# Optimization experiments

Hardware: AMD Instinct MI355X
Metric: run time of the kernel (lower is better)

The kernel has to match this reference:

```python
import jax, jax.numpy as jnp
import numpy as np

H = 1024       # hidden_size
I = 1024       # intermediate_size
E = 16         # num_experts
K = 4          # experts_per_token
LIMIT = 7.0    # swiglu_limit
ALPHA = 1.702  # swiglu alpha
EPS = 1e-5     # rmsnorm eps


def setup_inputs() -> dict:
    key = jax.random.key(0)
    ks = jax.random.split(key, 8)
    x = jax.random.normal(ks[0], (2, 512, H), dtype=jnp.float32)
    norm_scale = jnp.ones((H,), dtype=jnp.float32)
    wg = jax.random.normal(ks[1], (H, E), dtype=jnp.float32) * 0.02
    bg = jax.random.normal(ks[2], (E,), dtype=jnp.float32) * 0.02
    w1 = jax.random.normal(ks[3], (E, H, 2 * I), dtype=jnp.float32) * 0.02
    b1 = jax.random.normal(ks[4], (E, 2 * I), dtype=jnp.float32) * 0.02
    w2 = jax.random.normal(ks[5], (E, I, H), dtype=jnp.float32) * 0.02
    b2 = jax.random.normal(ks[6], (E, H), dtype=jnp.float32) * 0.02
    return {"x": x, "norm_scale": norm_scale, "wg": wg, "bg": bg,
            "w1": w1, "b1": b1, "w2": w2, "b2": b2}


def reference(x, norm_scale, wg, bg, w1, b1, w2, b2):
    shape = x.shape
    xf = x.reshape(-1, shape[-1])                                   # [T, H]
    # RMSNorm (float32 math)
    xn = xf * jax.lax.rsqrt(jnp.mean(xf * xf, axis=-1, keepdims=True) + EPS) * norm_scale
    # router logits + top-k with softmax over selected logits
    logits = xn @ wg + bg                                           # [T, E]
    vals, idx = jax.lax.top_k(logits, K)                            # [T, K]
    gates = jax.nn.softmax(vals, axis=-1)                           # [T, K]
    # dense [T, E] gate matrix (exactly equivalent to gather/scatter grouped GEMM)
    gate_full = jnp.einsum('tke,tk->te', jax.nn.one_hot(idx, E, dtype=gates.dtype), gates)
    # expert FFN 1 + fused swiglu (interleaved gate/linear pairs)
    h = jnp.einsum('th,ehd->etd', xn, w1) + b1[:, None, :]          # [E, T, 2I]
    a = jnp.minimum(h[..., ::2], LIMIT)                             # gate branch
    b = jnp.clip(h[..., 1::2], -LIMIT, LIMIT)                       # linear branch
    s = a * jax.nn.sigmoid(ALPHA * a) * (b + 1.0)                   # [E, T, I]
    # expert FFN 2; gamma (gate) scales the full epilogue incl. bias
    y = jnp.einsum('eti,eih->eth', s, w2) + b2[:, None, :]          # [E, T, H]
    t = jnp.einsum('eth,te->th', y, gate_full)                      # scatter-combine
    return x + t.reshape(shape)
```

## Files before the change

kernel.cpp:

```cpp
#include <hip/hip_runtime.h>

#define NH 1024
#define NI2 2048
#define NI 1024
#define NE 16
#define NT 1024

static constexpr float LIMITF = 7.0f;
static constexpr float ALPHAF = 1.702f;
static constexpr float EPSF = 1e-5f;

typedef short bf16x8 __attribute__((ext_vector_type(8)));
typedef float f32x16 __attribute__((ext_vector_type(16)));

__device__ __forceinline__ unsigned short f2bf(float f) {
  unsigned int u = __builtin_bit_cast(unsigned int, f);
  u = (u + 0x7FFFu + ((u >> 16) & 1u)) >> 16;
  return (unsigned short)u;
}

__global__ __launch_bounds__(256) void k_init(const float* __restrict__ x,
                                              float* __restrict__ out) {
  int i = blockIdx.x * 256 + threadIdx.x;
  reinterpret_cast<float4*>(out)[i] = reinterpret_cast<const float4*>(x)[i];
}

__global__ __launch_bounds__(256) void k_norm_router(
    const float* __restrict__ x, const float* __restrict__ nsc,
    const float* __restrict__ wg, const float* __restrict__ bg,
    unsigned short* __restrict__ xn, int* __restrict__ topk_idx,
    float* __restrict__ topk_gate, int* __restrict__ counts) {
  int t = blockIdx.x;
  int tid = threadIdx.x;
  int wave = tid >> 6, lane = tid & 63;

  float4 v = reinterpret_cast<const float4*>(x + (size_t)t * NH)[tid];
  float ss = v.x * v.x + v.y * v.y + v.z * v.z + v.w * v.w;
  for (int off = 32; off; off >>= 1) ss += __shfl_xor(ss, off);

  __shared__ float red[4];
  __shared__ float redl[4][16];
  __shared__ float logits_s[16];
  if (lane == 0) red[wave] = ss;
  __syncthreads();
  float tot = red[0] + red[1] + red[2] + red[3];
  float r = rsqrtf(tot * (1.0f / NH) + EPSF);

  float4 sc = reinterpret_cast<const float4*>(nsc)[tid];
  float xv[4];
  xv[0] = v.x * r * sc.x;
  xv[1] = v.y * r * sc.y;
  xv[2] = v.z * r * sc.z;
  xv[3] = v.w * r * sc.w;

  ushort4 o;
  o.x = f2bf(xv[0]); o.y = f2bf(xv[1]); o.z = f2bf(xv[2]); o.w = f2bf(xv[3]);
  reinterpret_cast<ushort4*>(xn + (size_t)t * NH)[tid] = o;

  float acc[16];
#pragma unroll
  for (int e = 0; e < 16; e++) acc[e] = 0.f;
  int hbase = tid * 4;
#pragma unroll
  for (int i = 0; i < 4; i++) {
    const float4* wr = reinterpret_cast<const float4*>(wg + (size_t)(hbase + i) * NE);
#pragma unroll
    for (int j = 0; j < 4; j++) {
      float4 w = wr[j];
      acc[j * 4 + 0] += xv[i] * w.x;
      acc[j * 4 + 1] += xv[i] * w.y;
      acc[j * 4 + 2] += xv[i] * w.z;
      acc[j * 4 + 3] += xv[i] * w.w;
    }
  }
#pragma unroll
  for (int e = 0; e < 16; e++)
    for (int off = 32; off; off >>= 1) acc[e] += __shfl_xor(acc[e], off);
  if (lane == 0) {
#pragma unroll
    for (int e = 0; e < 16; e++) redl[wave][e] = acc[e];
  }
  __syncthreads();
  if (tid < 16)
    logits_s[tid] = redl[0][tid] + redl[1][tid] + redl[2][tid] + redl[3][tid] + bg[tid];
  __syncthreads();

  if (tid == 0) {
    float vals[16];
#pragma unroll
    for (int e = 0; e < 16; e++) vals[e] = logits_s[e];
    int sel[4]; float sv[4];
    unsigned used = 0;
    for (int k = 0; k < 4; k++) {
      float best = -1e30f; int bi = 0;
      for (int e = 0; e < 16; e++) {
        if (!((used >> e) & 1u) && vals[e] > best) { best = vals[e]; bi = e; }
      }
      used |= 1u << bi; sel[k] = bi; sv[k] = best;
    }
    float g[4], ssum = 0.f;
    for (int k = 0; k < 4; k++) { g[k] = __expf(sv[k] - sv[0]); ssum += g[k]; }
    for (int k = 0; k < 4; k++) {
      topk_idx[t * 4 + k] = sel[k];
      topk_gate[t * 4 + k] = g[k] / ssum;
      atomicAdd(&counts[sel[k]], 1);
    }
  }
}

__global__ void k_scan(const int* __restrict__ counts, int* __restrict__ offsets,
                       int* __restrict__ cursor) {
  if (blockIdx.x == 0 && threadIdx.x == 0) {
    int o = 0;
    for (int e = 0; e < NE; e++) { offsets[e] = o; cursor[e] = o; o += counts[e]; }
  }
}

__global__ __launch_bounds__(256) void k_fill(const int* __restrict__ topk_idx,
                                              const float* __restrict__ topk_gate,
                                              int* __restrict__ cursor,
                                              int* __restrict__ rows_tok,
                                              float* __restrict__ rows_gate) {
  int idx = blockIdx.x * 256 + threadIdx.x;
  if (idx >= NT * 4) return;
  int e = topk_idx[idx];
  int slot = atomicAdd(&cursor[e], 1);
  rows_tok[slot] = idx >> 2;
  rows_gate[slot] = topk_gate[idx];
}

__global__ __launch_bounds__(256, 4) void k_ffn1(
    const unsigned short* __restrict__ xn, const float* __restrict__ w1,
    const float* __restrict__ b1, const int* __restrict__ counts,
    const int* __restrict__ offsets, const int* __restrict__ rows_tok,
    unsigned short* __restrict__ s_buf) {
  int e = blockIdx.y;
  int cnt = counts[e];
  if (cnt == 0) return;
  int n0 = blockIdx.x * 32;
  int rowbase = offsets[e];
  int tid = threadIdx.x;

  __shared__ __align__(16) unsigned short lds_b[2 * 16 * 32 * 8];

  const float* w1e = w1 + (size_t)e * (NH * NI2) + n0;
  int col = tid & 31, kc8 = tid >> 5;

  int lane = tid & 63, wave = tid >> 6;
  int lrow = lane & 31, khalf = lane >> 5;
  float bias = b1[(size_t)e * NI2 + n0 + lrow];
  int parity = lrow & 1;

  for (int m0 = 0; m0 < cnt; m0 += 256) {
    int tb0 = m0 + wave * 32;
    int tb1 = m0 + 128 + wave * 32;
    bool dual = (m0 + 128) < cnt;
    int tok0 = rows_tok[rowbase + min(tb0 + lrow, cnt - 1)];
    const unsigned short* a0p = xn + (size_t)tok0 * NH;
    const unsigned short* a1p = a0p;
    if (dual) {
      int tok1 = rows_tok[rowbase + min(tb1 + lrow, cnt - 1)];
      a1p = xn + (size_t)tok1 * NH;
    }

    f32x16 acc0 = {0.f,0.f,0.f,0.f,0.f,0.f,0.f,0.f,0.f,0.f,0.f,0.f,0.f,0.f,0.f,0.f};
    f32x16 acc1 = {0.f,0.f,0.f,0.f,0.f,0.f,0.f,0.f,0.f,0.f,0.f,0.f,0.f,0.f,0.f,0.f};

    __syncthreads();
#pragma unroll
    for (int half = 0; half < 2; half++) {
      int kcz = kc8 + half * 8;
      int kb = kcz * 8;
      float f[8];
#pragma unroll
      for (int j = 0; j < 8; j++) f[j] = w1e[(size_t)(kb + j) * NI2 + col];
      unsigned pk[4];
#pragma unroll
      for (int j = 0; j < 4; j++)
        pk[j] = (unsigned)f2bf(f[2 * j]) | ((unsigned)f2bf(f[2 * j + 1]) << 16);
      *reinterpret_cast<uint4*>(&lds_b[(size_t)(kcz * 32 + col) * 8]) =
          *reinterpret_cast<const uint4*>(pk);
    }
    __syncthreads();

    int buf = 0;
    for (int kt = 0; kt < 8; kt++) {
      float fst[2][8];
      if (kt < 7) {
        int k0n = (kt + 1) * 128;
#pragma unroll
        for (int half = 0; half < 2; half++) {
          int kb = (kc8 + half * 8) * 8;
#pragma unroll
          for (int j = 0; j < 8; j++)
            fst[half][j] = w1e[(size_t)(k0n + kb + j) * NI2 + col];
        }
      }
      const unsigned short* ab0 = a0p + kt * 128 + khalf * 8;
      const unsigned short* ab1 = a1p + kt * 128 + khalf * 8;
#pragma unroll
      for (int k2 = 0; k2 < 8; k2++) {
        bf16x8 bv = *reinterpret_cast<const bf16x8*>(
            &lds_b[(size_t)(((buf * 16) + k2 * 2 + khalf) * 32 + lrow) * 8]);
        bf16x8 av0 = *reinterpret_cast<const bf16x8*>(ab0 + k2 * 16);
        acc0 = __builtin_amdgcn_mfma_f32_32x32x16_bf16(av0, bv, acc0, 0, 0, 0);
        if (dual) {
          bf16x8 av1 = *reinterpret_cast<const bf16x8*>(ab1 + k2 * 16);
          acc1 = __builtin_amdgcn_mfma_f32_32x32x16_bf16(av1, bv, acc1, 0, 0, 0);
        }
      }
      if (kt < 7) {
        int nb = buf ^ 1;
#pragma unroll
        for (int half = 0; half < 2; half++) {
          int kcz = kc8 + half * 8;
          unsigned pk[4];
#pragma unroll
          for (int j = 0; j < 4; j++)
            pk[j] = (unsigned)f2bf(fst[half][2 * j]) |
                    ((unsigned)f2bf(fst[half][2 * j + 1]) << 16);
          *reinterpret_cast<uint4*>(
              &lds_b[(size_t)((nb * 16 + kcz) * 32 + col) * 8]) =
              *reinterpret_cast<const uint4*>(pk);
        }
        __syncthreads();
        buf = nb;
      }
    }

#pragma unroll
    for (int t2 = 0; t2 < 2; t2++) {
      if (t2 == 1 && !dual) break;
      f32x16 acc = t2 ? acc1 : acc0;
      int tb = t2 ? tb1 : tb0;
#pragma unroll
      for (int reg = 0; reg < 16; reg++) {
        float v = acc[reg] + bias;
        float p = __shfl_xor(v, 1);
        int row = (reg & 3) + 8 * (reg >> 2) + 4 * khalf;
        int m = tb + row;
        if (!parity && m < cnt) {
          float aa = fminf(v, LIMITF);
          float bb = fminf(fmaxf(p, -LIMITF), LIMITF);
          float sig = 1.0f / (1.0f + __expf(-ALPHAF * aa));
          float sval = aa * sig * (bb + 1.0f);
          s_buf[(size_t)(rowbase + m) * NI + ((n0 + lrow) >> 1)] = f2bf(sval);
        }
      }
    }
  }
}

__global__ __launch_bounds__(256, 4) void k_ffn2(
    const unsigned short* __restrict__ s_buf, const float* __restrict__ w2,
    const float* __restrict__ b2, const int* __restrict__ counts,
    const int* __restrict__ offsets, const int* __restrict__ rows_tok,
    const float* __restrict__ rows_gate, float* __restrict__ out) {
  int e = blockIdx.y;
  int cnt = counts[e];
  if (cnt == 0) return;
  int n0 = blockIdx.x * 32;
  int ks = blockIdx.z;
  int rowbase = offsets[e];
  int tid = threadIdx.x;

  __shared__ __align__(16) unsigned short lds_b[2 * 16 * 32 * 8];

  const float* w2e = w2 + (size_t)e * (NI * NH) + n0;
  int col = tid & 31, kc8 = tid >> 5;
  int kbase = ks * 512;

  int lane = tid & 63, wave = tid >> 6;
  int lrow = lane & 31, khalf = lane >> 5;
  float b2v = (ks == 0) ? b2[(size_t)e * NH + n0 + lrow] : 0.f;

  for (int m0 = 0; m0 < cnt; m0 += 256) {
    int tb0 = m0 + wave * 32;
    int tb1 = m0 + 128 + wave * 32;
    bool dual = (m0 + 128) < cnt;
    int r0 = rowbase + min(tb0 + lrow, cnt - 1);
    const unsigned short* a0p = s_buf + (size_t)r0 * NI + kbase;
    const unsigned short* a1p = a0p;
    if (dual) {
      int r1 = rowbase + min(tb1 + lrow, cnt - 1);
      a1p = s_buf + (size_t)r1 * NI + kbase;
    }

    f32x16 acc0 = {0.f,0.f,0.f,0.f,0.f,0.f,0.f,0.f,0.f,0.f,0.f,0.f,0.f,0.f,0.f,0.f};
    f32x16 acc1 = {0.f,0.f,0.f,0.f,0.f,0.f,0.f,0.f,0.f,0.f,0.f,0.f,0.f,0.f,0.f,0.f};

    __syncthreads();
#pragma unroll
    for (int half = 0; half < 2; half++) {
      int kcz = kc8 + half * 8;
      int kb = kcz * 8;
      float f[8];
#pragma unroll
      for (int j = 0; j < 8; j++)
        f[j] = w2e[(size_t)(kbase + kb + j) * NH + col];
      unsigned pk[4];
#pragma unroll
      for (int j = 0; j < 4; j++)
        pk[j] = (unsigned)f2bf(f[2 * j]) | ((unsigned)f2bf(f[2 * j + 1]) << 16);
      *reinterpret_cast<uint4*>(&lds_b[(size_t)(kcz * 32 + col) * 8]) =
          *reinterpret_cast<const uint4*>(pk);
    }
    __syncthreads();

    int buf = 0;
    for (int kt = 0; kt < 4; kt++) {
      float fst[2][8];
      if (kt < 3) {
        int k0n = kbase + (kt + 1) * 128;
#pragma unroll
        for (int half = 0; half < 2; half++) {
          int kb = (kc8 + half * 8) * 8;
#pragma unroll
          for (int j = 0; j < 8; j++)
            fst[half][j] = w2e[(size_t)(k0n + kb + j) * NH + col];
        }
      }
      const unsigned short* ab0 = a0p + kt * 128 + khalf * 8;
      const unsigned short* ab1 = a1p + kt * 128 + khalf * 8;
#pragma unroll
      for (int k2 = 0; k2 < 8; k2++) {
        bf16x8 bv = *reinterpret_cast<const bf16x8*>(
            &lds_b[(size_t)(((buf * 16) + k2 * 2 + khalf) * 32 + lrow) * 8]);
        bf16x8 av0 = *reinterpret_cast<const bf16x8*>(ab0 + k2 * 16);
        acc0 = __builtin_amdgcn_mfma_f32_32x32x16_bf16(av0, bv, acc0, 0, 0, 0);
        if (dual) {
          bf16x8 av1 = *reinterpret_cast<const bf16x8*>(ab1 + k2 * 16);
          acc1 = __builtin_amdgcn_mfma_f32_32x32x16_bf16(av1, bv, acc1, 0, 0, 0);
        }
      }
      if (kt < 3) {
        int nb = buf ^ 1;
#pragma unroll
        for (int half = 0; half < 2; half++) {
          int kcz = kc8 + half * 8;
          unsigned pk[4];
#pragma unroll
          for (int j = 0; j < 4; j++)
            pk[j] = (unsigned)f2bf(fst[half][2 * j]) |
                    ((unsigned)f2bf(fst[half][2 * j + 1]) << 16);
          *reinterpret_cast<uint4*>(
              &lds_b[(size_t)((nb * 16 + kcz) * 32 + col) * 8]) =
              *reinterpret_cast<const uint4*>(pk);
        }
        __syncthreads();
        buf = nb;
      }
    }

#pragma unroll
    for (int t2 = 0; t2 < 2; t2++) {
      if (t2 == 1 && !dual) break;
      f32x16 acc = t2 ? acc1 : acc0;
      int tb = t2 ? tb1 : tb0;
#pragma unroll
      for (int reg = 0; reg < 16; reg++) {
        int row = (reg & 3) + 8 * (reg >> 2) + 4 * khalf;
        int m = tb + row;
        if (m < cnt) {
          int rr = rowbase + m;
          int tok = rows_tok[rr];
          float g = rows_gate[rr];
          atomicAdd(&out[(size_t)tok * NH + n0 + lrow], g * (acc[reg] + b2v));
        }
      }
    }
  }
}

extern "C" void kernel_launch(void* const* d_in, const int* in_sizes, int n_in,
                              void* d_out, int out_size, void* d_ws, size_t ws_size,
                              hipStream_t stream) {
  const float* x   = (const float*)d_in[0];
  const float* nsc = (const float*)d_in[1];
  const float* wg  = (const float*)d_in[2];
  const float* bg  = (const float*)d_in[3];
  const float* w1  = (const float*)d_in[4];
  const float* b1  = (const float*)d_in[5];
  const float* w2  = (const float*)d_in[6];
  const float* b2  = (const float*)d_in[7];
  float* out = (float*)d_out;
  char* ws = (char*)d_ws;

  int*   counts    = (int*)(ws + 0);
  int*   offsets   = (int*)(ws + 64);
  int*   cursor    = (int*)(ws + 128);
  int*   topk_idx  = (int*)(ws + 1024);
  float* topk_gate = (float*)(ws + 1024 + 16384);
  int*   rows_tok  = (int*)(ws + 1024 + 32768);
  float* rows_gate = (float*)(ws + 1024 + 49152);
  unsigned short* xn    = (unsigned short*)(ws + 131072);
  unsigned short* s_buf = (unsigned short*)(ws + 4 * 1024 * 1024);

  hipMemsetAsync(ws, 0, 256, stream);
  k_init<<<NT * NH / 1024, 256, 0, stream>>>(x, out);
  k_norm_router<<<NT, 256, 0, stream>>>(x, nsc, wg, bg, xn, topk_idx, topk_gate,
                                        counts);
  k_scan<<<1, 64, 0, stream>>>(counts, offsets, cursor);
  k_fill<<<16, 256, 0, stream>>>(topk_idx, topk_gate, cursor, rows_tok, rows_gate);
  k_ffn1<<<dim3(NI2 / 32, NE), 256, 0, stream>>>(xn, w1, b1, counts, offsets,
                                                 rows_tok, s_buf);
  k_ffn2<<<dim3(NH / 32, NE, 2), 256, 0, stream>>>(s_buf, w2, b2, counts, offsets,
                                                   rows_tok, rows_gate, out);
}
```

Baseline: 472.6 us.

## Pack routed activations into MFMA-fragment tiles and replace atomic scatter with combine

Pads each expert's row range to multiples of 32 and gathers routed xn rows into a pre-swizzled fragment layout. Each lane then loads contiguous 16-byte A operands instead of gathering from scattered token rows. FFN1 writes the swiglu output through LDS into the same packed layout. FFN2 drops its split-K and atomicAdd scatter, writing gated per-slot outputs that a separate combine kernel sums with the residual. This removes the atomics and the init copy, at the cost of extra pack, pad and combine kernels plus intermediate buffer traffic and less FFN2 parallelism.

After: 457.8 us. 1.03x faster.

```diff
diff --git a/kernel.cpp b/kernel.cpp
--- a/kernel.cpp
+++ b/kernel.cpp
@@ -5,6 +5,8 @@
 #define NI 1024
 #define NE 16
 #define NT 1024
+#define MAXSLOT 4608
+#define MAXTILE 144
 
 static constexpr float LIMITF = 7.0f;
 static constexpr float ALPHAF = 1.702f;
@@ -17,12 +19,6 @@
   unsigned int u = __builtin_bit_cast(unsigned int, f);
   u = (u + 0x7FFFu + ((u >> 16) & 1u)) >> 16;
   return (unsigned short)u;
-}
-
-__global__ __launch_bounds__(256) void k_init(const float* __restrict__ x,
-                                              float* __restrict__ out) {
-  int i = blockIdx.x * 256 + threadIdx.x;
-  reinterpret_cast<float4*>(out)[i] = reinterpret_cast<const float4*>(x)[i];
 }
 
 __global__ __launch_bounds__(256) void k_norm_router(
@@ -112,7 +108,11 @@
                        int* __restrict__ cursor) {
   if (blockIdx.x == 0 && threadIdx.x == 0) {
     int o = 0;
-    for (int e = 0; e < NE; e++) { offsets[e] = o; cursor[e] = o; o += counts[e]; }
+    for (int e = 0; e < NE; e++) {
+      offsets[e] = o; cursor[e] = o;
+      o += (counts[e] + 31) & ~31;
+    }
+    offsets[NE] = o;
   }
 }
 
@@ -120,28 +120,62 @@
                                               const float* __restrict__ topk_gate,
                                               int* __restrict__ cursor,
                                               int* __restrict__ rows_tok,
-                                              float* __restrict__ rows_gate) {
+                                              float* __restrict__ rows_gate,
+                                              int* __restrict__ slot_of) {
   int idx = blockIdx.x * 256 + threadIdx.x;
   if (idx >= NT * 4) return;
   int e = topk_idx[idx];
   int slot = atomicAdd(&cursor[e], 1);
   rows_tok[slot] = idx >> 2;
   rows_gate[slot] = topk_gate[idx];
+  slot_of[idx] = slot;
+}
+
+__global__ void k_pad(const int* __restrict__ counts, const int* __restrict__ offsets,
+                      int* __restrict__ rows_tok, float* __restrict__ rows_gate) {
+  int e = blockIdx.x;
+  int start = offsets[e] + counts[e];
+  int end = offsets[e] + ((counts[e] + 31) & ~31);
+  int s = start + (int)threadIdx.x;
+  if (s < end) { rows_tok[s] = 0; rows_gate[s] = 0.f; }
+}
+
+__global__ __launch_bounds__(256) void k_pack(
+    const unsigned short* __restrict__ xn, const int* __restrict__ rows_tok,
+    const int* __restrict__ offsets, unsigned short* __restrict__ apack) {
+  int tile = blockIdx.x;
+  if (tile * 32 >= offsets[NE]) return;
+  int tid = threadIdx.x;
+  int r = tid >> 3, s = tid & 7;
+  int tok = rows_tok[tile * 32 + r];
+  const unsigned short* src = xn + (size_t)tok * NH;
+  int i0 = blockIdx.y * 4;
+#pragma unroll
+  for (int i = 0; i < 4; i++) {
+    int k0 = (i0 + i) * 64 + s * 8;
+    uint4 v = *reinterpret_cast<const uint4*>(src + k0);
+    int kstep = k0 >> 4;
+    int kh = s & 1;
+    *reinterpret_cast<uint4*>(
+        apack + ((size_t)(tile * 64 + kstep) * 64 + kh * 32 + r) * 8) = v;
+  }
 }
 
 __global__ __launch_bounds__(256, 4) void k_ffn1(
-    const unsigned short* __restrict__ xn, const float* __restrict__ w1,
+    const unsigned short* __restrict__ apack, const float* __restrict__ w1,
     const float* __restrict__ b1, const int* __restrict__ counts,
-    const int* __restrict__ offsets, const int* __restrict__ rows_tok,
-    unsigned short* __restrict__ s_buf) {
+    const int* __restrict__ offsets, unsigned short* __restrict__ spack) {
   int e = blockIdx.y;
   int cnt = counts[e];
   if (cnt == 0) return;
-  int n0 = blockIdx.x * 32;
-  int rowbase = offsets[e];
+  int ntiles = (cnt + 31) >> 5;
+  int tilebase = offsets[e] >> 5;
+  int bx = blockIdx.x;
+  int n0 = bx * 32;
   int tid = threadIdx.x;
 
   __shared__ __align__(16) unsigned short lds_b[2 * 16 * 32 * 8];
+  __shared__ __align__(16) unsigned short lds_t[4][32 * 16];
 
   const float* w1e = w1 + (size_t)e * (NH * NI2) + n0;
   int col = tid & 31, kc8 = tid >> 5;
@@ -151,17 +185,14 @@
   float bias = b1[(size_t)e * NI2 + n0 + lrow];
   int parity = lrow & 1;
 
-  for (int m0 = 0; m0 < cnt; m0 += 256) {
-    int tb0 = m0 + wave * 32;
-    int tb1 = m0 + 128 + wave * 32;
-    bool dual = (m0 + 128) < cnt;
-    int tok0 = rows_tok[rowbase + min(tb0 + lrow, cnt - 1)];
-    const unsigned short* a0p = xn + (size_t)tok0 * NH;
-    const unsigned short* a1p = a0p;
-    if (dual) {
-      int tok1 = rows_tok[rowbase + min(tb1 + lrow, cnt - 1)];
-      a1p = xn + (size_t)tok1 * NH;
-    }
+  for (int c0 = 0; c0 < ntiles; c0 += 8) {
+    int t0 = c0 + wave, t1 = c0 + wave + 4;
+    bool v0 = t0 < ntiles, v1 = t1 < ntiles;
+    int at0 = v0 ? t0 : 0, at1 = v1 ? t1 : 0;
+    const unsigned short* a0 =
+        apack + ((size_t)(tilebase + at0) * 64 * 64 + lane) * 8;
+    const unsigned short* a1 =
+        apack + ((size_t)(tilebase + at1) * 64 * 64 + lane) * 8;
 
     f32x16 acc0 = {0.f,0.f,0.f,0.f,0.f,0.f,0.f,0.f,0.f,0.f,0.f,0.f,0.f,0.f,0.f,0.f};
     f32x16 acc1 = {0.f,0.f,0.f,0.f,0.f,0.f,0.f,0.f,0.f,0.f,0.f,0.f,0.f,0.f,0.f,0.f};
@@ -196,18 +227,17 @@
             fst[half][j] = w1e[(size_t)(k0n + kb + j) * NI2 + col];
         }
       }
-      const unsigned short* ab0 = a0p + kt * 128 + khalf * 8;
-      const unsigned short* ab1 = a1p + kt * 128 + khalf * 8;
+      int ks0 = kt * 8;
 #pragma unroll
       for (int k2 = 0; k2 < 8; k2++) {
         bf16x8 bv = *reinterpret_cast<const bf16x8*>(
             &lds_b[(size_t)(((buf * 16) + k2 * 2 + khalf) * 32 + lrow) * 8]);
-        bf16x8 av0 = *reinterpret_cast<const bf16x8*>(ab0 + k2 * 16);
+        bf16x8 av0 =
+            *reinterpret_cast<const bf16x8*>(a0 + (size_t)(ks0 + k2) * 512);
         acc0 = __builtin_amdgcn_mfma_f32_32x32x16_bf16(av0, bv, acc0, 0, 0, 0);
-        if (dual) {
-          bf16x8 av1 = *reinterpret_cast<const bf16x8*>(ab1 + k2 * 16);
-          acc1 = __builtin_amdgcn_mfma_f32_32x32x16_bf16(av1, bv, acc1, 0, 0, 0);
-        }
+        bf16x8 av1 =
+            *reinterpret_cast<const bf16x8*>(a1 + (size_t)(ks0 + k2) * 512);
+        acc1 = __builtin_amdgcn_mfma_f32_32x32x16_bf16(av1, bv, acc1, 0, 0, 0);
       }
       if (kt < 7) {
         int nb = buf ^ 1;
@@ -230,61 +260,65 @@
 
 #pragma unroll
     for (int t2 = 0; t2 < 2; t2++) {
-      if (t2 == 1 && !dual) break;
+      bool vv = t2 ? v1 : v0;
+      int tt = t2 ? at1 : at0;
       f32x16 acc = t2 ? acc1 : acc0;
-      int tb = t2 ? tb1 : tb0;
+      __syncthreads();
 #pragma unroll
       for (int reg = 0; reg < 16; reg++) {
         float v = acc[reg] + bias;
         float p = __shfl_xor(v, 1);
-        int row = (reg & 3) + 8 * (reg >> 2) + 4 * khalf;
-        int m = tb + row;
-        if (!parity && m < cnt) {
+        if (!parity) {
           float aa = fminf(v, LIMITF);
           float bb = fminf(fmaxf(p, -LIMITF), LIMITF);
           float sig = 1.0f / (1.0f + __expf(-ALPHAF * aa));
           float sval = aa * sig * (bb + 1.0f);
-          s_buf[(size_t)(rowbase + m) * NI + ((n0 + lrow) >> 1)] = f2bf(sval);
-        }
+          int row = (reg & 3) + 8 * (reg >> 2) + 4 * khalf;
+          lds_t[wave][row * 16 + (lrow >> 1)] = f2bf(sval);
+        }
+      }
+      __syncthreads();
+      if (vv) {
+        bf16x8 frag = *reinterpret_cast<const bf16x8*>(
+            &lds_t[wave][(lane & 31) * 16 + (lane >> 5) * 8]);
+        *reinterpret_cast<bf16x8*>(
+            spack + ((size_t)((tilebase + tt) * 64 + bx) * 64 + lane) * 8) = frag;
       }
     }
   }
 }
 
 __global__ __launch_bounds__(256, 4) void k_ffn2(
-    const unsigned short* __restrict__ s_buf, const float* __restrict__ w2,
+    const unsigned short* __restrict__ spack, const float* __restrict__ w2,
     const float* __restrict__ b2, const int* __restrict__ counts,
-    const int* __restrict__ offsets, const int* __restrict__ rows_tok,
-    const float* __restrict__ rows_gate, float* __restrict__ out) {
+    const int* __restrict__ offsets, const float* __restrict__ rows_gate,
+    float* __restrict__ y_part) {
   int e = blockIdx.y;
   int cnt = counts[e];
   if (cnt == 0) return;
+  int ntiles = (cnt + 31) >> 5;
+  int tilebase = offsets[e] >> 5;
   int n0 = blockIdx.x * 32;
-  int ks = blockIdx.z;
-  int rowbase = offsets[e];
   int tid = threadIdx.x;
 
   __shared__ __align__(16) unsigned short lds_b[2 * 16 * 32 * 8];
+  __shared__ __align__(16) float lds_y[4][32 * 36];
 
   const float* w2e = w2 + (size_t)e * (NI * NH) + n0;
   int col = tid & 31, kc8 = tid >> 5;
-  int kbase = ks * 512;
 
   int lane = tid & 63, wave = tid >> 6;
   int lrow = lane & 31, khalf = lane >> 5;
-  float b2v = (ks == 0) ? b2[(size_t)e * NH + n0 + lrow] : 0.f;
-
-  for (int m0 = 0; m0 < cnt; m0 += 256) {
-    int tb0 = m0 + wave * 32;
-    int tb1 = m0 + 128 + wave * 32;
-    bool dual = (m0 + 128) < cnt;
-    int r0 = rowbase + min(tb0 + lrow, cnt - 1);
-    const unsigned short* a0p = s_buf + (size_t)r0 * NI + kbase;
-    const unsigned short* a1p = a0p;
-    if (dual) {
-      int r1 = rowbase + min(tb1 + lrow, cnt - 1);
-      a1p = s_buf + (size_t)r1 * NI + kbase;
-    }
+  float b2v = b2[(size_t)e * NH + n0 + lrow];
+
+  for (int c0 = 0; c0 < ntiles; c0 += 8) {
+    int t0 = c0 + wave, t1 = c0 + wave + 4;
+    bool v0 = t0 < ntiles, v1 = t1 < ntiles;
+    int at0 = v0 ? t0 : 0, at1 = v1 ? t1 : 0;
+    const unsigned short* a0 =
+        spack + ((size_t)(tilebase + at0) * 64 * 64 + lane) * 8;
+    const unsigned short* a1 =
+        spack + ((size_t)(tilebase + at1) * 64 * 64 + lane) * 8;
 
     f32x16 acc0 = {0.f,0.f,0.f,0.f,0.f,0.f,0.f,0.f,0.f,0.f,0.f,0.f,0.f,0.f,0.f,0.f};
     f32x16 acc1 = {0.f,0.f,0.f,0.f,0.f,0.f,0.f,0.f,0.f,0.f,0.f,0.f,0.f,0.f,0.f,0.f};
@@ -296,8 +330,7 @@
       int kb = kcz * 8;
       float f[8];
 #pragma unroll
-      for (int j = 0; j < 8; j++)
-        f[j] = w2e[(size_t)(kbase + kb + j) * NH + col];
+      for (int j = 0; j < 8; j++) f[j] = w2e[(size_t)(kb + j) * NH + col];
       unsigned pk[4];
 #pragma unroll
       for (int j = 0; j < 4; j++)
@@ -308,10 +341,10 @@
     __syncthreads();
 
     int buf = 0;
-    for (int kt = 0; kt < 4; kt++) {
+    for (int kt = 0; kt < 8; kt++) {
       float fst[2][8];
-      if (kt < 3) {
-        int k0n = kbase + (kt + 1) * 128;
+      if (kt < 7) {
+        int k0n = (kt + 1) * 128;
 #pragma unroll
         for (int half = 0; half < 2; half++) {
           int kb = (kc8 + half * 8) * 8;
@@ -320,20 +353,19 @@
             fst[half][j] = w2e[(size_t)(k0n + kb + j) * NH + col];
         }
       }
-      const unsigned short* ab0 = a0p + kt * 128 + khalf * 8;
-      const unsigned short* ab1 = a1p + kt * 128 + khalf * 8;
+      int ks0 = kt * 8;
 #pragma unroll
       for (int k2 = 0; k2 < 8; k2++) {
         bf16x8 bv = *reinterpret_cast<const bf16x8*>(
             &lds_b[(size_t)(((buf * 16) + k2 * 2 + khalf) * 32 + lrow) * 8]);
-        bf16x8 av0 = *reinterpret_cast<const bf16x8*>(ab0 + k2 * 16);
+        bf16x8 av0 =
+            *reinterpret_cast<const bf16x8*>(a0 + (size_t)(ks0 + k2) * 512);
         acc0 = __builtin_amdgcn_mfma_f32_32x32x16_bf16(av0, bv, acc0, 0, 0, 0);
-        if (dual) {
-          bf16x8 av1 = *reinterpret_cast<const bf16x8*>(ab1 + k2 * 16);
-          acc1 = __builtin_amdgcn_mfma_f32_32x32x16_bf16(av1, bv, acc1, 0, 0, 0);
-        }
-      }
-      if (kt < 3) {
+        bf16x8 av1 =
+            *reinterpret_cast<const bf16x8*>(a1 + (size_t)(ks0 + k2) * 512);
+        acc1 = __builtin_amdgcn_mfma_f32_32x32x16_bf16(av1, bv, acc1, 0, 0, 0);
+      }
+      if (kt < 7) {
         int nb = buf ^ 1;
 #pragma unroll
         for (int half = 0; half < 2; half++) {
@@ -354,22 +386,50 @@
 
 #pragma unroll
     for (int t2 = 0; t2 < 2; t2++) {
-      if (t2 == 1 && !dual) break;
+      bool vv = t2 ? v1 : v0;
+      int tt = t2 ? at1 : at0;
       f32x16 acc = t2 ? acc1 : acc0;
-      int tb = t2 ? tb1 : tb0;
+      __syncthreads();
 #pragma unroll
       for (int reg = 0; reg < 16; reg++) {
         int row = (reg & 3) + 8 * (reg >> 2) + 4 * khalf;
-        int m = tb + row;
-        if (m < cnt) {
-          int rr = rowbase + m;
-          int tok = rows_tok[rr];
-          float g = rows_gate[rr];
-          atomicAdd(&out[(size_t)tok * NH + n0 + lrow], g * (acc[reg] + b2v));
-        }
-      }
-    }
-  }
+        lds_y[wave][row * 36 + lrow] = acc[reg] + b2v;
+      }
+      __syncthreads();
+      if (vv) {
+        int row = lane & 31, ch = lane >> 5;
+        int slot = (tilebase + tt) * 32 + row;
+        float g = rows_gate[slot];
+        float* dst = y_part + (size_t)slot * NH + n0 + ch * 16;
+#pragma unroll
+        for (int q = 0; q < 4; q++) {
+          float4 yv =
+              *reinterpret_cast<const float4*>(&lds_y[wave][row * 36 + ch * 16 + q * 4]);
+          yv.x *= g; yv.y *= g; yv.z *= g; yv.w *= g;
+          reinterpret_cast<float4*>(dst)[q] = yv;
+        }
+      }
+    }
+  }
+}
+
+__global__ __launch_bounds__(256) void k_combine(
+    const float* __restrict__ x, const int* __restrict__ slot_of,
+    const float* __restrict__ y_part, float* __restrict__ out) {
+  int t = blockIdx.x;
+  int tid = threadIdx.x;
+  int s0 = slot_of[t * 4 + 0], s1 = slot_of[t * 4 + 1];
+  int s2 = slot_of[t * 4 + 2], s3 = slot_of[t * 4 + 3];
+  float4 r = reinterpret_cast<const float4*>(x + (size_t)t * NH)[tid];
+  float4 a = reinterpret_cast<const float4*>(y_part + (size_t)s0 * NH)[tid];
+  float4 b = reinterpret_cast<const float4*>(y_part + (size_t)s1 * NH)[tid];
+  float4 c = reinterpret_cast<const float4*>(y_part + (size_t)s2 * NH)[tid];
+  float4 d = reinterpret_cast<const float4*>(y_part + (size_t)s3 * NH)[tid];
+  r.x += a.x + b.x + c.x + d.x;
+  r.y += a.y + b.y + c.y + d.y;
+  r.z += a.z + b.z + c.z + d.z;
+  r.w += a.w + b.w + c.w + d.w;
+  reinterpret_cast<float4*>(out + (size_t)t * NH)[tid] = r;
 }
 
 extern "C" void kernel_launch(void* const* d_in, const int* in_sizes, int n_in,
@@ -387,23 +447,29 @@
   char* ws = (char*)d_ws;
 
   int*   counts    = (int*)(ws + 0);
-  int*   offsets   = (int*)(ws + 64);
-  int*   cursor    = (int*)(ws + 128);
-  int*   topk_idx  = (int*)(ws + 1024);
-  float* topk_gate = (float*)(ws + 1024 + 16384);
-  int*   rows_tok  = (int*)(ws + 1024 + 32768);
-  float* rows_gate = (float*)(ws + 1024 + 49152);
-  unsigned short* xn    = (unsigned short*)(ws + 131072);
-  unsigned short* s_buf = (unsigned short*)(ws + 4 * 1024 * 1024);
-
-  hipMemsetAsync(ws, 0, 256, stream);
-  k_init<<<NT * NH / 1024, 256, 0, stream>>>(x, out);
+  int*   offsets   = (int*)(ws + 128);
+  int*   cursor    = (int*)(ws + 256);
+  int*   slot_of   = (int*)(ws + 4096);
+  int*   topk_idx  = (int*)(ws + 20480);
+  float* topk_gate = (float*)(ws + 36864);
+  int*   rows_tok  = (int*)(ws + 53248);
+  float* rows_gate = (float*)(ws + 71680);
+  unsigned short* xn    = (unsigned short*)(ws + (1u << 20));
+  unsigned short* apack = (unsigned short*)(ws + (4u << 20));
+  unsigned short* spack = (unsigned short*)(ws + (16u << 20));
+  float*          y_part = (float*)(ws + (28u << 20));
+
+  hipMemsetAsync(ws, 0, 512, stream);
   k_norm_router<<<NT, 256, 0, stream>>>(x, nsc, wg, bg, xn, topk_idx, topk_gate,
                                         counts);
   k_scan<<<1, 64, 0, stream>>>(counts, offsets, cursor);
-  k_fill<<<16, 256, 0, stream>>>(topk_idx, topk_gate, cursor, rows_tok, rows_gate);
-  k_ffn1<<<dim3(NI2 / 32, NE), 256, 0, stream>>>(xn, w1, b1, counts, offsets,
-                                                 rows_tok, s_buf);
-  k_ffn2<<<dim3(NH / 32, NE, 2), 256, 0, stream>>>(s_buf, w2, b2, counts, offsets,
-                                                   rows_tok, rows_gate, out);
-}
+  k_fill<<<16, 256, 0, stream>>>(topk_idx, topk_gate, cursor, rows_tok, rows_gate,
+                                 slot_of);
+  k_pad<<<16, 32, 0, stream>>>(counts, offsets, rows_tok, rows_gate);
+  k_pack<<<dim3(MAXTILE, 4), 256, 0, stream>>>(xn, rows_tok, offsets, apack);
+  k_ffn1<<<dim3(NI2 / 32, NE), 256, 0, stream>>>(apack, w1, b1, counts, offsets,
+                                                 spack);
+  k_ffn2<<<dim3(NH / 32, NE), 256, 0, stream>>>(spack, w2, b2, counts, offsets,
+                                                rows_gate, y_part);
+  k_combine<<<NT, 256, 0, stream>>>(x, slot_of, y_part, out);
+}
```
